# Kernel optimization log

Hardware: AMD Instinct MI355X
Metric: run time of the kernel (lower is better)

## Reference

```python
import jax, jax.numpy as jnp
import numpy as np

PI = 3.141592653589793
DET_THRESHOLD = 0.25
MAX_DET = 100
REG_HEAD = 4
DEPTH_MEAN = 28.01  # smoke_coder.depth_ref[0]
DIM_REF = (3.88, 1.63, 1.53)  # smoke_coder.dim_ref[0] (l, h, w)


def setup_inputs() -> dict:
    key = jax.random.key(0)
    k1, k2, k3, k4 = jax.random.split(key, 4)
    B, C, H, W = 32, 3, 256, 832  # stride-4 feature map of 3328x1024 images
    pred_heatmap = jax.random.uniform(k1, (B, C, H, W), dtype=jnp.float32)
    pred_regression = jax.random.normal(k2, (B, C + 1, H, W), dtype=jnp.float32) * 0.1  # REG_HEAD=4 channels
    trans_mat = jnp.tile(jnp.array([[0.25, 0.0, 0.0], [0.0, 0.25, 0.0], [0.0, 0.0, 1.0]], jnp.float32), (B, 1, 1))
    K_mat = jnp.tile(jnp.array([[2100.0, 0.0, 1664.0], [0.0, 2100.0, 512.0], [0.0, 0.0, 1.0]], jnp.float32), (B, 1, 1))
    size = jnp.tile(jnp.array([3328.0, 1024.0], jnp.float32), (B, 1))  # (img_w, img_h)
    h_cam = jax.random.uniform(k3, (B,), jnp.float32, 1.4, 2.0)
    dimensions = jax.random.uniform(k4, (B, 3), jnp.float32, 1.5, 4.0)
    return dict(pred_heatmap=pred_heatmap, pred_regression=pred_regression, trans_mat=trans_mat,
                K_mat=K_mat, size=size, h_cam=h_cam, dimensions=dimensions)


def reference(pred_heatmap, pred_regression, trans_mat, K_mat, size, h_cam, dimensions):
    B, C, H, W = pred_heatmap.shape
    K = MAX_DET
    # ---- nms_hm: 3x3 max-pool, keep local maxima ----
    hmax = jax.lax.reduce_window(pred_heatmap, -jnp.inf, jax.lax.max, (1, 1, 3, 3), (1, 1, 1, 1), 'SAME')
    heat = pred_heatmap * (hmax == pred_heatmap).astype(pred_heatmap.dtype)
    # ---- select_topk: per-class topk then global topk ----
    scores_c, inds_c = jax.lax.top_k(heat.reshape(B, C, H * W), K)  # [B,C,K]
    ys_c = (inds_c // W).astype(jnp.float32)
    xs_c = (inds_c % W).astype(jnp.float32)
    scores, topk_ind = jax.lax.top_k(scores_c.reshape(B, C * K), K)  # [B,K]
    clses = (topk_ind // K).astype(jnp.float32)
    inds = jnp.take_along_axis(inds_c.reshape(B, C * K), topk_ind, axis=1)
    ys = jnp.take_along_axis(ys_c.reshape(B, C * K), topk_ind, axis=1)
    xs = jnp.take_along_axis(xs_c.reshape(B, C * K), topk_ind, axis=1)
    feat = pred_regression.reshape(B, REG_HEAD, H * W).transpose(0, 2, 1)  # [B,HW,R]
    pois = jnp.take_along_axis(feat, inds[:, :, None], axis=1).reshape(-1, REG_HEAD)  # [B*K,R]
    log_dv_delta = pois[:, 0]
    off_u = pois[:, 1]
    ori = pois[:, 2:]
    # ---- feature points -> image points via inverse affine ----
    pts = jnp.stack([xs.reshape(-1), ys.reshape(-1)], axis=1)
    pts = pts + jnp.stack([off_u, jnp.zeros_like(off_u)], axis=1)
    pts_h = jnp.concatenate([pts, jnp.ones((pts.shape[0], 1), pts.dtype)], axis=1)  # [N,3]
    obj = jnp.repeat(jnp.arange(B), K)
    trans_inv = jnp.linalg.inv(trans_mat)[obj]  # [N,3,3]
    img_pts = jnp.einsum('nij,nj->ni', trans_inv, pts_h)[:, :2]
    # ---- per-object camera params ----
    Ks = K_mat[obj]
    h = h_cam[obj]
    kd = dimensions[obj]
    fx, fy, cx = Ks[:, 0, 0], Ks[:, 1, 1], Ks[:, 0, 2]
    dim_ref = jnp.array(DIM_REF, jnp.float32)
    dims = jnp.where(jnp.isfinite(kd), kd, dim_ref[None, :])
    # ---- geometric depth decode ----
    h_ref = h - dims[:, 1] / 2.0
    log_dv_ref = jnp.log(jnp.clip(fy * jnp.abs(h_ref), 1e-7, None) / DEPTH_MEAN)
    log_dv = jnp.clip(log_dv_ref + log_dv_delta, -4.0, 8.0)
    depths = jnp.clip(fy * jnp.abs(h_ref) * jnp.exp(-log_dv), 0.5, 120.0)
    px = (img_pts[:, 0] - cx) * depths / fx
    locs = jnp.stack([px, h, depths], axis=1)  # [N,3]
    # ---- decode_orientation (SMOKE) ----
    rays = jnp.arctan(locs[:, 0] / (locs[:, 2] + 1e-7))
    alphas = jnp.arctan(ori[:, 0] / (ori[:, 1] + 1e-7))
    alphas = alphas + jnp.where(ori[:, 1] >= 0, -PI / 2, PI / 2)
    rotys = alphas + rays
    rotys = jnp.where(rotys > PI, rotys - 2 * PI, rotys)
    rotys = jnp.where(rotys < -PI, rotys + 2 * PI, rotys)
    # ---- encode_box2d: build 3D corners, rotate, project, clamp ----
    cos, sin = jnp.cos(rotys), jnp.sin(rotys)
    cx8 = jnp.array([-0.5, 0.5, 0.5, 0.5, 0.5, -0.5, -0.5, -0.5], jnp.float32)
    cy8 = jnp.array([-1.0, -1.0, 0.0, 0.0, -1.0, -1.0, 0.0, 0.0], jnp.float32)
    cz8 = jnp.array([-0.5, -0.5, -0.5, 0.5, 0.5, 0.5, 0.5, -0.5], jnp.float32)
    xc = dims[:, 0:1] * cx8  # l
    yc = dims[:, 1:2] * cy8  # h
    zc = dims[:, 2:3] * cz8  # w
    bx = cos[:, None] * xc + sin[:, None] * zc
    bz = -sin[:, None] * xc + cos[:, None] * zc
    box3d = jnp.stack([bx, yc, bz], axis=1) + locs[:, :, None]  # [N,3,8]
    proj = jnp.einsum('nij,njk->nik', Ks, box3d)
    uv = proj[:, :2, :] / proj[:, 2:3, :]
    img_w = size.reshape(-1)[0]
    img_h = size.reshape(-1)[1]
    xmins = jnp.clip(jnp.min(uv[:, 0, :], axis=1), 0.0, img_w)
    xmaxs = jnp.clip(jnp.max(uv[:, 0, :], axis=1), 0.0, img_w)
    ymins = jnp.clip(jnp.min(uv[:, 1, :], axis=1), 0.0, img_h)
    ymaxs = jnp.clip(jnp.max(uv[:, 1, :], axis=1), 0.0, img_h)
    box2d = jnp.stack([xmins, ymins, xmaxs, ymaxs], axis=1)
    pred_dims = jnp.roll(dims, -1, axis=1)  # (l,h,w)->(h,w,l)
    result = jnp.concatenate([clses.reshape(-1, 1), alphas[:, None], box2d, pred_dims, locs,
                              rotys[:, None], scores.reshape(-1, 1)], axis=1)  # [N,14]
    # fixed-shape equivalent of boolean filtering: zero out rows below threshold
    keep = (result[:, -1] > DET_THRESHOLD).astype(result.dtype)
    return result * keep[:, None]
```

## Files before the change

### kernel.cpp

```cpp
#include <hip/hip_runtime.h>
#include <math.h>

#define B_ 32
#define C_ 3
#define H_ 256
#define W_ 832
#define HW_ (H_*W_)
#define K_ 100
#define RPB 16
#define PARTS (H_/RPB)
#define NLOAD (W_/4)
#define BLK 256
#define CAP 2048
#define NCAND (C_*PARTS*K_)

typedef unsigned long long ull;
struct DetRec { float score; int cls; unsigned hw; };

template<int N>
__device__ inline void bitonic_sort_desc(ull* s) {
    for (int k = 2; k <= N; k <<= 1) {
        for (int j = k >> 1; j > 0; j >>= 1) {
            __syncthreads();
            for (int i = threadIdx.x; i < N; i += BLK) {
                int ixj = i ^ j;
                if (ixj > i) {
                    ull a = s[i], b = s[ixj];
                    bool up = ((i & k) == 0);
                    if (up ? (a < b) : (a > b)) { s[i] = b; s[ixj] = a; }
                }
            }
        }
    }
    __syncthreads();
}

__device__ ull radix_select(const ull* __restrict__ buf, int cnt, int k) {
    __shared__ unsigned hist[256];
    __shared__ ull pref_s;
    __shared__ int k_s;
    const int tid = threadIdx.x;
    if (cnt < k) return 0ULL;
    if (tid == 0) { pref_s = 0ULL; k_s = k; }
    __syncthreads();
    for (int pos = 7; pos >= 0; --pos) {
        hist[tid] = 0;
        __syncthreads();
        const ull prefix = pref_s;
        const int kk = k_s;
        for (int i = tid; i < cnt; i += BLK) {
            const ull key = buf[i];
            const bool match = (pos == 7) || ((key >> (8 * (pos + 1))) == prefix);
            if (match) atomicAdd(&hist[(unsigned)(key >> (8 * pos)) & 255u], 1u);
        }
        __syncthreads();
        for (int off = 1; off < 256; off <<= 1) {
            const unsigned add = (tid + off < 256) ? hist[tid + off] : 0u;
            __syncthreads();
            hist[tid] += add;
            __syncthreads();
        }
        const unsigned above = (tid == 255) ? 0u : hist[tid + 1];
        if (hist[tid] >= (unsigned)kk && above < (unsigned)kk) {
            pref_s = (prefix << 8) | (ull)tid;
            k_s = kk - (int)above;
        }
        __syncthreads();
    }
    return pref_s;
}

__global__ void __launch_bounds__(BLK) topk_part_kernel(
        const float* __restrict__ heat, ull* __restrict__ part_out) {
    const int chan = blockIdx.x / PARTS;
    const int c    = chan % C_;
    const int part = blockIdx.x % PARTS;
    const float* __restrict__ hp = heat + (size_t)chan * HW_;
    const int r0 = part * RPB;
    const int tid = threadIdx.x;
    const bool active = tid < NLOAD;
    const int x4 = tid * 4;
    const int lane = tid & 63;

    __shared__ float vmA[W_], vmB[W_];
    __shared__ ull buf[CAP];
    __shared__ int cnt;
    if (tid == 0) cnt = 0;

    float4 rA, rB, rC, rD;
    if (active) {
        const int ym1 = (r0 == 0) ? 0 : r0 - 1;
        rA = reinterpret_cast<const float4*>(hp + (size_t)ym1 * W_)[tid];
        rB = reinterpret_cast<const float4*>(hp + (size_t)r0  * W_)[tid];
        const int yp1 = (r0 == H_ - 1) ? r0 : r0 + 1;
        rC = reinterpret_cast<const float4*>(hp + (size_t)yp1 * W_)[tid];
    }
    __syncthreads();

    for (int r = 0; r < RPB; ++r) {
        const int y = r0 + r;
        float* vr = (r & 1) ? vmB : vmA;
        float4 vm;
        if (active) {
            const int yn = (y + 2 > H_ - 1) ? H_ - 1 : y + 2;
            rD = reinterpret_cast<const float4*>(hp + (size_t)yn * W_)[tid];
            vm.x = fmaxf(fmaxf(rA.x, rB.x), rC.x);
            vm.y = fmaxf(fmaxf(rA.y, rB.y), rC.y);
            vm.z = fmaxf(fmaxf(rA.z, rB.z), rC.z);
            vm.w = fmaxf(fmaxf(rA.w, rB.w), rC.w);
            reinterpret_cast<float4*>(&vr[x4])[0] = vm;
        }
        __syncthreads();
        {
            float left = -INFINITY, right = -INFINITY;
            float vv0 = 0.f, vv1 = 0.f, vv2 = 0.f, vv3 = 0.f;
            if (active) {
                left  = (tid == 0)         ? -INFINITY : vr[x4 - 1];
                right = (tid == NLOAD - 1) ? -INFINITY : vr[x4 + 4];
                vv0 = rB.x; vv1 = rB.y; vv2 = rB.z; vv3 = rB.w;
            }
            const float vn[6] = {left, vm.x, vm.y, vm.z, vm.w, right};
            const float vv[4] = {vv0, vv1, vv2, vv3};
            #pragma unroll
            for (int i = 0; i < 4; ++i) {
                const float v = vv[i];
                const bool peak = active && (v >= vn[i]) && (v >= vn[i+1]) && (v >= vn[i+2]);
                const ull m = __ballot(peak);
                if (peak) {
                    const unsigned p = (unsigned)(y * W_ + x4 + i);
                    const unsigned tie = ((unsigned)c << 18) | p;
                    const ull key = ((ull)__float_as_uint(v) << 32) | (ull)(~tie);
                    const int rank = __popcll(m & ((1ULL << lane) - 1ULL));
                    const int leader = __ffsll((long long)m) - 1;
                    int base = 0;
                    if (lane == leader) base = atomicAdd(&cnt, (int)__popcll(m));
                    base = __shfl(base, leader);
                    const int pos = base + rank;
                    if (pos < CAP) buf[pos] = key;
                }
            }
        }
        rA = rB; rB = rC; rC = rD;
    }
    __syncthreads();

    const int cc = (cnt < CAP) ? cnt : CAP;
    const ull thr = radix_select(buf, cc, K_);

    __shared__ int ocnt;
    if (tid == 0) ocnt = 0;
    __syncthreads();
    ull* o = part_out + (size_t)blockIdx.x * K_;
    for (int i = tid; i < cc; i += BLK) {
        const ull key = buf[i];
        if (key >= thr && key != 0ULL) {
            const int p = atomicAdd(&ocnt, 1);
            if (p < K_) o[p] = key;
        }
    }
    __syncthreads();
    const int oc = (ocnt < K_) ? ocnt : K_;
    for (int i = oc + tid; i < K_; i += BLK) o[i] = 0ULL;
}

__global__ void __launch_bounds__(BLK) merge_kernel(
        const ull* __restrict__ part_keys, DetRec* __restrict__ dets) {
    const int b = blockIdx.x;
    const int tid = threadIdx.x;
    __shared__ ull buf[NCAND];
    __shared__ ull sel[128];
    __shared__ int ocnt;
    const ull* src = part_keys + (size_t)b * NCAND;
    for (int i = tid; i < NCAND; i += BLK) buf[i] = src[i];
    if (tid < 128) sel[tid] = 0ULL;
    if (tid == 0) ocnt = 0;
    __syncthreads();

    const ull thr = radix_select(buf, NCAND, K_);
    for (int i = tid; i < NCAND; i += BLK) {
        const ull key = buf[i];
        if (key >= thr && key != 0ULL) {
            const int p = atomicAdd(&ocnt, 1);
            if (p < 128) sel[p] = key;
        }
    }
    bitonic_sort_desc<128>(sel);

    for (int i = tid; i < K_; i += BLK) {
        const ull key = sel[i];
        const unsigned tie = ~(unsigned)(key & 0xFFFFFFFFULL);
        DetRec d;
        d.score = __uint_as_float((unsigned)(key >> 32));
        d.cls   = (int)((tie >> 18) & 3u);
        d.hw    = tie & 0x3FFFFu;
        dets[(size_t)b * K_ + i] = d;
    }
}

__global__ void __launch_bounds__(BLK) geom_kernel(
        const DetRec* __restrict__ dets, const float* __restrict__ reg,
        const float* __restrict__ trans, const float* __restrict__ Km,
        const float* __restrict__ sz, const float* __restrict__ hcam,
        const float* __restrict__ dimen, float* __restrict__ out) {
    const int n = blockIdx.x * blockDim.x + threadIdx.x;
    if (n >= B_ * K_) return;
    const int b = n / K_;
    DetRec d = dets[n];
    const float score = d.score;
    const float clsf = (float)d.cls;
    unsigned hw = d.hw; if (hw >= HW_) hw = 0;
    const float xs = (float)(hw % W_);
    const float ys = (float)(hw / W_);

    const float* rg = reg + (size_t)b * 4 * HW_;
    const float delta = rg[hw];
    const float off_u = rg[HW_ + hw];
    const float ori0  = rg[2 * HW_ + hw];
    const float ori1  = rg[3 * HW_ + hw];

    const float* T = trans + b * 9;
    const float t00=T[0], t01=T[1], t02=T[2], t10=T[3], t11=T[4], t12=T[5],
                t20=T[6], t21=T[7], t22=T[8];
    const float det3 = t00*(t11*t22 - t12*t21) - t01*(t10*t22 - t12*t20)
                     + t02*(t10*t21 - t11*t20);
    const float idt = 1.0f / det3;
    const float i00 = (t11*t22 - t12*t21)*idt;
    const float i01 = (t02*t21 - t01*t22)*idt;
    const float i02 = (t01*t12 - t02*t11)*idt;

    const float pu = xs + off_u;
    const float img_x = i00*pu + i01*ys + i02;

    const float* Kb = Km + b * 9;
    const float k00=Kb[0],k01=Kb[1],k02=Kb[2],k10=Kb[3],k11=Kb[4],k12=Kb[5],
                k20=Kb[6],k21=Kb[7],k22=Kb[8];
    const float fx = k00, fy = k11, cx = k02;
    const float h = hcam[b];
    float d0 = dimen[b*3+0], d1 = dimen[b*3+1], d2 = dimen[b*3+2];
    if (!isfinite(d0)) d0 = 3.88f;
    if (!isfinite(d1)) d1 = 1.63f;
    if (!isfinite(d2)) d2 = 1.53f;

    const float h_ref = h - d1 * 0.5f;
    const float fyh = fy * fabsf(h_ref);
    const float log_dv_ref = logf(fmaxf(fyh, 1e-7f) / 28.01f);
    const float log_dv = fminf(fmaxf(log_dv_ref + delta, -4.0f), 8.0f);
    const float depth = fminf(fmaxf(fyh * expf(-log_dv), 0.5f), 120.0f);
    const float px = (img_x - cx) * depth / fx;

    const float PI_F  = 3.14159265358979323846f;
    const float ray = atanf(px / (depth + 1e-7f));
    float alpha = atanf(ori0 / (ori1 + 1e-7f));
    alpha += (ori1 >= 0.0f) ? -1.5707963267948966f : 1.5707963267948966f;
    float roty = alpha + ray;
    if (roty >  PI_F) roty -= 6.283185307179586f;
    if (roty < -PI_F) roty += 6.283185307179586f;

    const float cosr = cosf(roty), sinr = sinf(roty);
    const float cx8[8] = {-0.5f, 0.5f, 0.5f, 0.5f, 0.5f,-0.5f,-0.5f,-0.5f};
    const float cy8[8] = {-1.0f,-1.0f, 0.0f, 0.0f,-1.0f,-1.0f, 0.0f, 0.0f};
    const float cz8[8] = {-0.5f,-0.5f,-0.5f, 0.5f, 0.5f, 0.5f, 0.5f,-0.5f};
    float umin = 1e30f, umax = -1e30f, vmin = 1e30f, vmax = -1e30f;
    #pragma unroll
    for (int i = 0; i < 8; ++i) {
        const float xc = d0 * cx8[i];
        const float yc = d1 * cy8[i];
        const float zc = d2 * cz8[i];
        const float X = cosr*xc + sinr*zc + px;
        const float Y = yc + h;
        const float Z = -sinr*xc + cosr*zc + depth;
        const float w = k20*X + k21*Y + k22*Z;
        const float u = (k00*X + k01*Y + k02*Z) / w;
        const float v = (k10*X + k11*Y + k12*Z) / w;
        umin = fminf(umin, u); umax = fmaxf(umax, u);
        vmin = fminf(vmin, v); vmax = fmaxf(vmax, v);
    }
    const float img_w = sz[0], img_h = sz[1];
    const float xmin = fminf(fmaxf(umin, 0.0f), img_w);
    const float xmax = fminf(fmaxf(umax, 0.0f), img_w);
    const float ymin = fminf(fmaxf(vmin, 0.0f), img_h);
    const float ymax = fminf(fmaxf(vmax, 0.0f), img_h);

    const float keep = (score > 0.25f) ? 1.0f : 0.0f;
    float* o = out + (size_t)n * 14;
    o[0]  = clsf  * keep;
    o[1]  = alpha * keep;
    o[2]  = xmin  * keep;
    o[3]  = ymin  * keep;
    o[4]  = xmax  * keep;
    o[5]  = ymax  * keep;
    o[6]  = d1    * keep;
    o[7]  = d2    * keep;
    o[8]  = d0    * keep;
    o[9]  = px    * keep;
    o[10] = h     * keep;
    o[11] = depth * keep;
    o[12] = roty  * keep;
    o[13] = score * keep;
}

extern "C" void kernel_launch(void* const* d_in, const int* in_sizes, int n_in,
                              void* d_out, int out_size, void* d_ws, size_t ws_size,
                              hipStream_t stream) {
    const float* heat  = (const float*)d_in[0];
    const float* reg   = (const float*)d_in[1];
    const float* trans = (const float*)d_in[2];
    const float* Kmat  = (const float*)d_in[3];
    const float* sz    = (const float*)d_in[4];
    const float* hcam  = (const float*)d_in[5];
    const float* dimen = (const float*)d_in[6];
    float* out = (float*)d_out;

    char* ws = (char*)d_ws;
    ull* part_keys = (ull*)ws;
    ws += (size_t)B_ * C_ * PARTS * K_ * sizeof(ull);
    DetRec* dets = (DetRec*)ws;

    topk_part_kernel<<<B_ * C_ * PARTS, BLK, 0, stream>>>(heat, part_keys);
    merge_kernel<<<B_, BLK, 0, stream>>>(part_keys, dets);
    geom_kernel<<<(B_ * K_ + BLK - 1) / BLK, BLK, 0, stream>>>(
        dets, reg, trans, Kmat, sz, hcam, dimen, out);
}
```

Before: 262.5 us.

## Fuse merge and geometry kernels; use wave-aggregated atomics and shuffle scans in radix select

Merges the merge and geom kernels into one launch, so the DetRec workspace round-trip and one kernel launch go away. Radix select now groups histogram atomics by wave leader and replaces the LDS Hillis-Steele scan, which had many barriers, with a wave-shuffle suffix scan. Candidate compaction uses ballot/popcount so each wave issues a single atomic instead of one per thread. The cost is that geometry now runs on only 32 blocks of 100 active threads, which reduces its parallelism.

```diff
diff --git a/kernel.cpp b/kernel.cpp
--- a/kernel.cpp
+++ b/kernel.cpp
@@ -15,7 +15,6 @@
 #define NCAND (C_*PARTS*K_)
 
 typedef unsigned long long ull;
-struct DetRec { float score; int cls; unsigned hw; };
 
 template<int N>
 __device__ inline void bitonic_sort_desc(ull* s) {
@@ -37,36 +36,61 @@
 
 __device__ ull radix_select(const ull* __restrict__ buf, int cnt, int k) {
     __shared__ unsigned hist[256];
+    __shared__ unsigned wsum[4];
     __shared__ ull pref_s;
     __shared__ int k_s;
     const int tid = threadIdx.x;
+    const int lane = tid & 63;
+    const int wv = tid >> 6;
     if (cnt < k) return 0ULL;
     if (tid == 0) { pref_s = 0ULL; k_s = k; }
-    __syncthreads();
+
     for (int pos = 7; pos >= 0; --pos) {
+        __syncthreads();
         hist[tid] = 0;
         __syncthreads();
         const ull prefix = pref_s;
         const int kk = k_s;
-        for (int i = tid; i < cnt; i += BLK) {
-            const ull key = buf[i];
-            const bool match = (pos == 7) || ((key >> (8 * (pos + 1))) == prefix);
-            if (match) atomicAdd(&hist[(unsigned)(key >> (8 * pos)) & 255u], 1u);
-        }
-        __syncthreads();
-        for (int off = 1; off < 256; off <<= 1) {
-            const unsigned add = (tid + off < 256) ? hist[tid + off] : 0u;
-            __syncthreads();
-            hist[tid] += add;
-            __syncthreads();
-        }
-        const unsigned above = (tid == 255) ? 0u : hist[tid + 1];
-        if (hist[tid] >= (unsigned)kk && above < (unsigned)kk) {
+        for (int i0 = 0; i0 < cnt; i0 += BLK) {
+            const int i = i0 + tid;
+            ull key = (i < cnt) ? buf[i] : 0ULL;
+            bool todo = (i < cnt) &&
+                        ((pos == 7) || ((key >> (8 * (pos + 1))) == prefix));
+            unsigned d = (unsigned)(key >> (8 * pos)) & 255u;
+            #pragma unroll
+            for (int it = 0; it < 4; ++it) {
+                const ull act = __ballot(todo);
+                if (act == 0ULL) break;
+                const int leader = __ffsll((long long)act) - 1;
+                const unsigned dl = (unsigned)__shfl((int)d, leader);
+                const bool same = todo && (d == dl);
+                const ull ms = __ballot(same);
+                if (lane == leader) atomicAdd(&hist[dl], (unsigned)__popcll(ms));
+                if (same) todo = false;
+            }
+            if (todo) atomicAdd(&hist[d], 1u);
+        }
+        __syncthreads();
+        const unsigned h = hist[tid];
+        unsigned v = h;
+        #pragma unroll
+        for (int off = 1; off < 64; off <<= 1) {
+            const unsigned o = __shfl_down(v, off);
+            if (lane + off < 64) v += o;
+        }
+        if (lane == 0) wsum[wv] = v;
+        __syncthreads();
+        unsigned carry = 0;
+        #pragma unroll
+        for (int w = 0; w < 4; ++w) if (w > wv) carry += wsum[w];
+        const unsigned S = v + carry;
+        const unsigned above = S - h;
+        if (S >= (unsigned)kk && above < (unsigned)kk) {
             pref_s = (prefix << 8) | (ull)tid;
             k_s = kk - (int)above;
         }
-        __syncthreads();
-    }
+    }
+    __syncthreads();
     return pref_s;
 }
 
@@ -151,64 +175,63 @@
     if (tid == 0) ocnt = 0;
     __syncthreads();
     ull* o = part_out + (size_t)blockIdx.x * K_;
-    for (int i = tid; i < cc; i += BLK) {
-        const ull key = buf[i];
-        if (key >= thr && key != 0ULL) {
-            const int p = atomicAdd(&ocnt, 1);
-            if (p < K_) o[p] = key;
-        }
+    for (int i0 = 0; i0 < cc; i0 += BLK) {
+        const int i = i0 + tid;
+        const ull key = (i < cc) ? buf[i] : 0ULL;
+        const bool sel = (i < cc) && (key >= thr) && (key != 0ULL);
+        const ull m = __ballot(sel);
+        const int nsel = (int)__popcll(m);
+        int base = 0;
+        if (lane == 0 && nsel) base = atomicAdd(&ocnt, nsel);
+        base = __shfl(base, 0);
+        const int rank = (int)__popcll(m & ((1ULL << lane) - 1ULL));
+        if (sel && base + rank < K_) o[base + rank] = key;
     }
     __syncthreads();
     const int oc = (ocnt < K_) ? ocnt : K_;
     for (int i = oc + tid; i < K_; i += BLK) o[i] = 0ULL;
 }
 
-__global__ void __launch_bounds__(BLK) merge_kernel(
-        const ull* __restrict__ part_keys, DetRec* __restrict__ dets) {
+__global__ void __launch_bounds__(BLK) merge_geom_kernel(
+        const ull* __restrict__ part_keys, const float* __restrict__ reg,
+        const float* __restrict__ trans, const float* __restrict__ Km,
+        const float* __restrict__ sz, const float* __restrict__ hcam,
+        const float* __restrict__ dimen, float* __restrict__ out) {
     const int b = blockIdx.x;
     const int tid = threadIdx.x;
+    const int lane = tid & 63;
     __shared__ ull buf[NCAND];
-    __shared__ ull sel[128];
+    __shared__ ull sel_s[128];
     __shared__ int ocnt;
     const ull* src = part_keys + (size_t)b * NCAND;
     for (int i = tid; i < NCAND; i += BLK) buf[i] = src[i];
-    if (tid < 128) sel[tid] = 0ULL;
+    if (tid < 128) sel_s[tid] = 0ULL;
     if (tid == 0) ocnt = 0;
     __syncthreads();
 
     const ull thr = radix_select(buf, NCAND, K_);
-    for (int i = tid; i < NCAND; i += BLK) {
-        const ull key = buf[i];
-        if (key >= thr && key != 0ULL) {
-            const int p = atomicAdd(&ocnt, 1);
-            if (p < 128) sel[p] = key;
-        }
-    }
-    bitonic_sort_desc<128>(sel);
-
-    for (int i = tid; i < K_; i += BLK) {
-        const ull key = sel[i];
-        const unsigned tie = ~(unsigned)(key & 0xFFFFFFFFULL);
-        DetRec d;
-        d.score = __uint_as_float((unsigned)(key >> 32));
-        d.cls   = (int)((tie >> 18) & 3u);
-        d.hw    = tie & 0x3FFFFu;
-        dets[(size_t)b * K_ + i] = d;
-    }
-}
-
-__global__ void __launch_bounds__(BLK) geom_kernel(
-        const DetRec* __restrict__ dets, const float* __restrict__ reg,
-        const float* __restrict__ trans, const float* __restrict__ Km,
-        const float* __restrict__ sz, const float* __restrict__ hcam,
-        const float* __restrict__ dimen, float* __restrict__ out) {
-    const int n = blockIdx.x * blockDim.x + threadIdx.x;
-    if (n >= B_ * K_) return;
-    const int b = n / K_;
-    DetRec d = dets[n];
-    const float score = d.score;
-    const float clsf = (float)d.cls;
-    unsigned hw = d.hw; if (hw >= HW_) hw = 0;
+    for (int i0 = 0; i0 < NCAND; i0 += BLK) {
+        const int i = i0 + tid;
+        const ull key = (i < NCAND) ? buf[i] : 0ULL;
+        const bool sel = (i < NCAND) && (key >= thr) && (key != 0ULL);
+        const ull m = __ballot(sel);
+        const int nsel = (int)__popcll(m);
+        int base = 0;
+        if (lane == 0 && nsel) base = atomicAdd(&ocnt, nsel);
+        base = __shfl(base, 0);
+        const int rank = (int)__popcll(m & ((1ULL << lane) - 1ULL));
+        if (sel && base + rank < 128) sel_s[base + rank] = key;
+    }
+    bitonic_sort_desc<128>(sel_s);
+
+    if (tid >= K_) return;
+    const int n = b * K_ + tid;
+    const ull key = sel_s[tid];
+    const unsigned tie = ~(unsigned)(key & 0xFFFFFFFFULL);
+    const float score = __uint_as_float((unsigned)(key >> 32));
+    const float clsf  = (float)((tie >> 18) & 3u);
+    unsigned hw = tie & 0x3FFFFu;
+    if (hw >= HW_) hw = 0;
     const float xs = (float)(hw % W_);
     const float ys = (float)(hw / W_);
 
@@ -248,7 +271,7 @@
     const float depth = fminf(fmaxf(fyh * expf(-log_dv), 0.5f), 120.0f);
     const float px = (img_x - cx) * depth / fx;
 
-    const float PI_F  = 3.14159265358979323846f;
+    const float PI_F = 3.14159265358979323846f;
     const float ray = atanf(px / (depth + 1e-7f));
     float alpha = atanf(ori0 / (ori1 + 1e-7f));
     alpha += (ori1 >= 0.0f) ? -1.5707963267948966f : 1.5707963267948966f;
@@ -311,13 +334,9 @@
     const float* dimen = (const float*)d_in[6];
     float* out = (float*)d_out;
 
-    char* ws = (char*)d_ws;
-    ull* part_keys = (ull*)ws;
-    ws += (size_t)B_ * C_ * PARTS * K_ * sizeof(ull);
-    DetRec* dets = (DetRec*)ws;
+    ull* part_keys = (ull*)d_ws;
 
     topk_part_kernel<<<B_ * C_ * PARTS, BLK, 0, stream>>>(heat, part_keys);
-    merge_kernel<<<B_, BLK, 0, stream>>>(part_keys, dets);
-    geom_kernel<<<(B_ * K_ + BLK - 1) / BLK, BLK, 0, stream>>>(
-        dets, reg, trans, Kmat, sz, hcam, dimen, out);
-}
+    merge_geom_kernel<<<B_, BLK, 0, stream>>>(
+        part_keys, reg, trans, Kmat, sz, hcam, dimen, out);
+}
```

Result: slower. 268.1 us (+2.2%).
